# Optimization experiments

Measured on AMD Instinct MI355X. Metric: run time of the kernel, lower is better.

## Reference

```python
import jax, jax.numpy as jnp
import numpy as np

B, N, D = 64, 1024, 128
K = 6  # hardcoded neighbor count in the module


def setup_inputs() -> dict:
    key = jax.random.key(0)
    ks = jax.random.split(key, 11)
    def lin(k, out_d, in_d):
        kw, kb = jax.random.split(k)
        s = 1.0 / np.sqrt(in_d)
        W = jax.random.uniform(kw, (out_d, in_d), minval=-s, maxval=s, dtype=jnp.float32)
        b = jax.random.uniform(kb, (out_d,), minval=-s, maxval=s, dtype=jnp.float32)
        return W, b
    loc = jax.random.uniform(ks[0], (B, N, 2), dtype=jnp.float32)
    deadline = jax.random.uniform(ks[1], (B, N), dtype=jnp.float32)
    depot = jax.random.uniform(ks[2], (B, 2), dtype=jnp.float32)
    W3d, b3d = lin(ks[3], D, 3)
    W2d, b2d = lin(ks[4], D, 2)
    Wnb, bnb = lin(ks[5], D, K * D)
    Wdep, bdep = lin(ks[6], D, 2)
    return {"loc": loc, "deadline": deadline, "depot": depot,
            "W3d": W3d, "b3d": b3d, "W2d": W2d, "b2d": b2d,
            "Wnb": Wnb, "bnb": bnb, "Wdep": Wdep, "bdep": bdep}


def reference(loc, deadline, depot, W3d, b3d, W2d, b2d, Wnb, bnb, Wdep, bdep):
    x = jnp.concatenate([loc, deadline[:, :, None]], axis=2)  # [B,N,3]
    x2 = x[:, :, 0:2]                                          # [B,N,2]
    F2 = jnp.einsum('bnf,df->bnd', x2, W2d) + b2d              # [B,N,D]
    F3 = jnp.einsum('bnf,df->bnd', x, W3d) + b3d               # [B,N,D]
    # pairwise euclidean distances; indices are non-differentiable -> stop_gradient
    diff = x2[:, None, :, :] - x2[:, :, None, :]               # [B,N,N,2]
    dist = jnp.sqrt(jnp.sum(diff * diff, axis=-1))             # [B,N,N]
    _, neighbors = jax.lax.top_k(jax.lax.stop_gradient(-dist), K)  # [B,N,K] smallest dists (incl. self)
    # faithful quirk: original does F0_embedding_2d[:, neighbors][0] == gather from batch-0 embeddings
    nb = F2[0][neighbors]                                      # [B,N,K,D]
    nb_c = nb.reshape(nb.shape[0], nb.shape[1], K * nb.shape[3])  # [B,N,K*D]
    Fn = jnp.einsum('bnf,df->bnd', nb_c, Wnb) + bnb            # [B,N,D]
    Ff = Fn + F3
    dep = depot @ Wdep.T + bdep                                 # [B,D]
    h = jax.nn.leaky_relu(jnp.concatenate([dep[:, None, :], Ff], axis=1), negative_slope=0.01)
    return h, h.mean(axis=1)
```

## Files before the change

### kernel.cpp

```cpp
#include <hip/hip_runtime.h>
#include <hip/hip_bf16.h>

#define CB 64
#define CN 1024
#define CD 128
#define CK 6

typedef __attribute__((ext_vector_type(8))) short short8;
typedef __attribute__((ext_vector_type(4))) float floatx4;

__device__ __forceinline__ unsigned short f2bf(float f) {
    union { float f; unsigned u; } c; c.f = f;
    unsigned u = c.u;
    u += 0x7FFFu + ((u >> 16) & 1u);
    return (unsigned short)(u >> 16);
}

#define WS_F2B    0
#define WS_WNBB   262144
#define WS_PART   458752
#define WS_NBRS   983040
#define WS_IDS    1769472
#define WS_STARTS 1900544

__global__ void __launch_bounds__(256) k_grid(
    const float* __restrict__ loc,
    const float* __restrict__ W2d,
    const float* __restrict__ b2d,
    const float* __restrict__ Wnb,
    unsigned short* __restrict__ ids,
    int* __restrict__ starts,
    unsigned short* __restrict__ F2b,
    unsigned short* __restrict__ Wnbb)
{
    __shared__ float2 pts[CN];
    __shared__ int cnt[256];
    __shared__ int base[256];
    int b = blockIdx.x, t = threadIdx.x;
    const float2* lb = (const float2*)loc + b * CN;
#pragma unroll
    for (int r = 0; r < 4; ++r) pts[t + r * 256] = lb[t + r * 256];
    cnt[t] = 0;
    __syncthreads();
    int mycell[4];
#pragma unroll
    for (int r = 0; r < 4; ++r) {
        float2 p = pts[t * 4 + r];
        int cx = (int)(p.x * 16.0f); cx = cx > 15 ? 15 : cx;
        int cy = (int)(p.y * 16.0f); cy = cy > 15 ? 15 : cy;
        mycell[r] = (cy << 4) + cx;
        atomicAdd(&cnt[mycell[r]], 1);
    }
    __syncthreads();
    for (int off = 1; off < 256; off <<= 1) {
        int u = (t >= off) ? cnt[t - off] : 0;
        __syncthreads();
        cnt[t] += u;
        __syncthreads();
    }
    int excl = (t == 0) ? 0 : cnt[t - 1];
    base[t] = excl;
    starts[b * 257 + t] = excl;
    if (t == 255) starts[b * 257 + 256] = cnt[255];
    __syncthreads();
#pragma unroll
    for (int r = 0; r < 4; ++r) {
        int pos = atomicAdd(&base[mycell[r]], 1);
        ids[b * CN + pos] = (unsigned short)(t * 4 + r);
    }
#pragma unroll
    for (int e = 0; e < 8; ++e) {
        int idx = b * 2048 + e * 256 + t;
        int n = idx >> 7, d = idx & 127;
        float v = fmaf(loc[n * 2], W2d[d * 2],
                  fmaf(loc[n * 2 + 1], W2d[d * 2 + 1], b2d[d]));
        F2b[idx] = f2bf(v);
    }
#pragma unroll
    for (int e = 0; e < 6; ++e) {
        int idx = b * 1536 + e * 256 + t;
        Wnbb[idx] = f2bf(Wnb[idx]);
    }
}

__global__ void __launch_bounds__(256) k_knn(
    const float* __restrict__ loc,
    const unsigned short* __restrict__ ids,
    const int* __restrict__ starts,
    unsigned short* __restrict__ nbrs)
{
    __shared__ float2 xy_tmp[CN];
    __shared__ float2 xy_s[CN];
    __shared__ unsigned short ids_s[CN];
    __shared__ int st_s[257];
    int t = threadIdx.x;
    int b = blockIdx.x >> 2;
    int qbase = (blockIdx.x & 3) << 8;
    const float2* lb = (const float2*)loc + b * CN;
#pragma unroll
    for (int r = 0; r < 4; ++r) {
        int p = t + r * 256;
        xy_tmp[p] = lb[p];
        ids_s[p] = ids[b * CN + p];
    }
    st_s[t] = starts[b * 257 + t];
    if (t == 0) st_s[256] = starts[b * 257 + 256];
    __syncthreads();
#pragma unroll
    for (int r = 0; r < 4; ++r) {
        int p = t + r * 256;
        xy_s[p] = xy_tmp[ids_s[p]];
    }
    __syncthreads();

    int qp = qbase + t;
    int q = ids_s[qp];
    float2 qxy = xy_s[qp];
    float xq = qxy.x, yq = qxy.y;
    int cx = (int)(xq * 16.0f); cx = cx > 15 ? 15 : cx;
    int cy = (int)(yq * 16.0f); cy = cy > 15 ? 15 : cy;
    float dk[CK]; int ik[CK];
#pragma unroll
    for (int s = 0; s < CK; ++s) { dk[s] = 1e30f; ik[s] = 0x7FFFFFFF; }
    float dk5sq = __builtin_inff();
    const float h = 0.0625f;

#define KNN_CAND(P)                                                        \
    {                                                                      \
        float2 v = xy_s[P];                                                \
        float dx = __fsub_rn(v.x, xq);                                     \
        float dy = __fsub_rn(v.y, yq);                                     \
        float d2 = __fadd_rn(__fmul_rn(dx, dx), __fmul_rn(dy, dy));        \
        if (d2 < dk5sq) {                                                  \
            float ds = __fsqrt_rn(d2);                                     \
            int j = ids_s[P];                                              \
            if (ds < dk[CK - 1] || (ds == dk[CK - 1] && j < ik[CK - 1])) { \
                float dc = ds; int jc = j;                                 \
                _Pragma("unroll")                                          \
                for (int s = 0; s < CK; ++s) {                             \
                    bool sw = (dc < dk[s]) || (dc == dk[s] && jc < ik[s]); \
                    float od = dk[s]; int oi = ik[s];                      \
                    dk[s] = sw ? dc : od; ik[s] = sw ? jc : oi;            \
                    dc = sw ? od : dc;    jc = sw ? oi : jc;               \
                }                                                          \
                if (ik[CK - 1] != 0x7FFFFFFF)                              \
                    dk5sq = __fmul_rn(dk[CK - 1], dk[CK - 1]) * 1.000001f; \
            }                                                              \
        }                                                                  \
    }

    {
        int yl = cy > 0 ? cy - 1 : 0, yh = cy < 15 ? cy + 1 : 15;
        int xl = cx > 0 ? cx - 1 : 0, xh = cx < 15 ? cx + 1 : 15;
        for (int yy = yl; yy <= yh; ++yy) {
            int p  = st_s[(yy << 4) + xl];
            int pe = st_s[(yy << 4) + xh + 1];
            for (; p < pe; ++p) KNN_CAND(p)
        }
    }
    bool done;
    {
        int x0 = cx - 1, x1 = cx + 1, y0 = cy - 1, y1 = cy + 1;
        done = (x0 <= 0 && y0 <= 0 && x1 >= 15 && y1 >= 15);
        float mL = x0 > 0  ? __fsub_rn(xq, (float)x0 * h)       : 1e30f;
        float mR = x1 < 15 ? __fsub_rn((float)(x1 + 1) * h, xq) : 1e30f;
        float mB = y0 > 0  ? __fsub_rn(yq, (float)y0 * h)       : 1e30f;
        float mT = y1 < 15 ? __fsub_rn((float)(y1 + 1) * h, yq) : 1e30f;
        float bound = fminf(fminf(mL, mR), fminf(mB, mT)) * 0.999999f;
        done = done || (ik[CK - 1] != 0x7FFFFFFF && dk[CK - 1] < bound);
    }
    if (!done) {
        for (int r = 2; r < 16; ++r) {
            int x0 = cx - r, x1 = cx + r, y0 = cy - r, y1 = cy + r;
            int yl = y0 < 0 ? 0 : y0, yh = y1 > 15 ? 15 : y1;
            int xl = x0 < 0 ? 0 : x0, xh = x1 > 15 ? 15 : x1;
            for (int yy = yl; yy <= yh; ++yy) {
                bool ey = (yy == y0) || (yy == y1);
                if (ey) {
                    int p  = st_s[(yy << 4) + xl];
                    int pe = st_s[(yy << 4) + xh + 1];
                    for (; p < pe; ++p) KNN_CAND(p)
                } else {
                    if (x0 >= 0) {
                        int p  = st_s[(yy << 4) + x0];
                        int pe = st_s[(yy << 4) + x0 + 1];
                        for (; p < pe; ++p) KNN_CAND(p)
                    }
                    if (x1 <= 15) {
                        int p  = st_s[(yy << 4) + x1];
                        int pe = st_s[(yy << 4) + x1 + 1];
                        for (; p < pe; ++p) KNN_CAND(p)
                    }
                }
            }
            if (x0 <= 0 && y0 <= 0 && x1 >= 15 && y1 >= 15) break;
            float mL = x0 > 0  ? __fsub_rn(xq, (float)x0 * h)       : 1e30f;
            float mR = x1 < 15 ? __fsub_rn((float)(x1 + 1) * h, xq) : 1e30f;
            float mB = y0 > 0  ? __fsub_rn(yq, (float)y0 * h)       : 1e30f;
            float mT = y1 < 15 ? __fsub_rn((float)(y1 + 1) * h, yq) : 1e30f;
            float bound = fminf(fminf(mL, mR), fminf(mB, mT)) * 0.999999f;
            if (ik[CK - 1] != 0x7FFFFFFF && dk[CK - 1] < bound) break;
        }
    }
#undef KNN_CAND
    unsigned short* o = nbrs + (unsigned)(b * CN + q) * CK;
#pragma unroll
    for (int s = 0; s < CK; ++s) o[s] = (unsigned short)ik[s];
}

__global__ void __launch_bounds__(256) k_gemm(
    const float* __restrict__ loc,
    const float* __restrict__ dl,
    const unsigned short* __restrict__ F2b,
    const unsigned short* __restrict__ Wnbb,
    const unsigned short* __restrict__ nbrs,
    const float* __restrict__ bnb,
    const float* __restrict__ W3d,
    const float* __restrict__ b3d,
    float* __restrict__ outh,
    float* __restrict__ partials)
{
    __shared__ unsigned short As[128 * 40];
    __shared__ unsigned short Bs[128 * 40];
    __shared__ float psum[4][CD];

    int t = threadIdx.x;
    int rowbase = blockIdx.x * 128;
    int bb = rowbase >> 10;

    int ar0 = t >> 2, aseg = t & 3;
    int nb0[CK], nb1[CK];
#pragma unroll
    for (int s = 0; s < CK; ++s) {
        nb0[s] = (int)nbrs[(rowbase + ar0) * CK + s];
        nb1[s] = (int)nbrs[(rowbase + ar0 + 64) * CK + s];
    }

    int wave = t >> 6, lane = t & 63;
    int koff = (lane >> 4) * 8;
    int mrow = lane & 15;
    int bd = t >> 1, bhalf = t & 1;

    floatx4 acc[2][8];
#pragma unroll
    for (int i = 0; i < 2; ++i)
#pragma unroll
        for (int j = 0; j < 8; ++j) acc[i][j] = (floatx4){0.f, 0.f, 0.f, 0.f};

#pragma unroll
    for (int c = 0; c < 24; ++c) {
        const int kk = c >> 2;
        const int inner = (c & 3) * 32;
        __syncthreads();
        *(uint4*)&As[ar0 * 40 + aseg * 8] =
            *(const uint4*)(F2b + nb0[kk] * 128 + inner + aseg * 8);
        *(uint4*)&As[(ar0 + 64) * 40 + aseg * 8] =
            *(const uint4*)(F2b + nb1[kk] * 128 + inner + aseg * 8);
        {
            const uint4* src = (const uint4*)(Wnbb + bd * 768 + c * 32 + bhalf * 16);
            *(uint4*)&Bs[bd * 40 + bhalf * 16] = src[0];
            *(uint4*)&Bs[bd * 40 + bhalf * 16 + 8] = src[1];
        }
        __syncthreads();
        short8 af[2];
#pragma unroll
        for (int i = 0; i < 2; ++i)
            af[i] = *(const short8*)&As[(wave * 32 + i * 16 + mrow) * 40 + koff];
#pragma unroll
        for (int j = 0; j < 8; ++j) {
            short8 bfr = *(const short8*)&Bs[(j * 16 + mrow) * 40 + koff];
#pragma unroll
            for (int i = 0; i < 2; ++i)
                acc[i][j] = __builtin_amdgcn_mfma_f32_16x16x32_bf16(
                    af[i], bfr, acc[i][j], 0, 0, 0);
        }
    }

    int lq = lane >> 4, lc = lane & 15;
    float rl0[8], rl1[8], rdl[8]; int rn[8];
#pragma unroll
    for (int ir = 0; ir < 8; ++ir) {
        int i = ir >> 2, r = ir & 3;
        int mg = rowbase + wave * 32 + i * 16 + lq * 4 + r;
        float2 l2 = ((const float2*)loc)[mg];
        rl0[ir] = l2.x; rl1[ir] = l2.y; rdl[ir] = dl[mg];
        rn[ir] = mg & 1023;
    }
#pragma unroll
    for (int j = 0; j < 8; ++j) {
        int d = j * 16 + lc;
        float w0 = W3d[d * 3], w1 = W3d[d * 3 + 1], w2 = W3d[d * 3 + 2];
        float bias = b3d[d] + bnb[d];
        float csum = 0.f;
#pragma unroll
        for (int ir = 0; ir < 8; ++ir) {
            int i = ir >> 2, r = ir & 3;
            float v = acc[i][j][r] + bias + rl0[ir] * w0 + rl1[ir] * w1 + rdl[ir] * w2;
            float lr = v >= 0.f ? v : 0.01f * v;
            outh[((long)bb * 1025 + rn[ir] + 1) * 128 + d] = lr;
            csum += lr;
        }
        csum += __shfl_xor(csum, 16);
        csum += __shfl_xor(csum, 32);
        if (lq == 0) psum[wave][d] = csum;
    }
    __syncthreads();
    if (t < CD)
        partials[blockIdx.x * 128 + t] =
            psum[0][t] + psum[1][t] + psum[2][t] + psum[3][t];
}

__global__ void k_fin(const float* __restrict__ depot,
                      const float* __restrict__ Wdep,
                      const float* __restrict__ bdep,
                      const float* __restrict__ partials,
                      float* __restrict__ out) {
    int idx = blockIdx.x * 256 + threadIdx.x;
    int b = idx >> 7, d = idx & 127;
    float acc = 0.f;
#pragma unroll
    for (int g = 0; g < 8; ++g) acc += partials[(b * 8 + g) * 128 + d];
    float dv = depot[b * 2] * Wdep[d * 2] + depot[b * 2 + 1] * Wdep[d * 2 + 1] + bdep[d];
    float lr = dv >= 0.f ? dv : 0.01f * dv;
    out[(long)b * 1025 * 128 + d] = lr;
    out[(long)CB * 1025 * 128 + idx] = (acc + lr) * (1.0f / 1025.0f);
}

extern "C" void kernel_launch(void* const* d_in, const int* in_sizes, int n_in,
                              void* d_out, int out_size, void* d_ws, size_t ws_size,
                              hipStream_t stream) {
    const float* loc      = (const float*)d_in[0];
    const float* deadline = (const float*)d_in[1];
    const float* depot    = (const float*)d_in[2];
    const float* W3d      = (const float*)d_in[3];
    const float* b3d      = (const float*)d_in[4];
    const float* W2d      = (const float*)d_in[5];
    const float* b2d      = (const float*)d_in[6];
    const float* Wnb      = (const float*)d_in[7];
    const float* bnb      = (const float*)d_in[8];
    const float* Wdep     = (const float*)d_in[9];
    const float* bdep     = (const float*)d_in[10];
    float* out = (float*)d_out;

    char* ws = (char*)d_ws;
    unsigned short* F2b   = (unsigned short*)(ws + WS_F2B);
    unsigned short* Wnbb  = (unsigned short*)(ws + WS_WNBB);
    float* partials       = (float*)(ws + WS_PART);
    unsigned short* nbrs  = (unsigned short*)(ws + WS_NBRS);
    unsigned short* ids   = (unsigned short*)(ws + WS_IDS);
    int* starts           = (int*)(ws + WS_STARTS);

    k_grid<<<64, 256, 0, stream>>>(loc, W2d, b2d, Wnb, ids, starts, F2b, Wnbb);
    k_knn<<<256, 256, 0, stream>>>(loc, ids, starts, nbrs);
    k_gemm<<<512, 256, 0, stream>>>(loc, deadline, F2b, Wnbb, nbrs, bnb,
                                    W3d, b3d, out, partials);
    k_fin<<<32, 256, 0, stream>>>(depot, Wdep, bdep, partials, out);
}
```

Measured before the change: 142.9 us.

## Split each kNN query across four lanes and merge top-k via shuffles

Each query point is now handled by four threads rather than one. Each thread scans every fourth candidate in the grid cells and keeps its own top-6, and the four partial lists are merged with xor shuffles. The grid grows from 256 to 1024 blocks to raise occupancy and parallelism on the kNN search. The cost is that every block reloads the whole batch's coordinates into shared memory, each lane prunes with a weaker per-lane bound, lanes may expand to different search rings, and there is extra merge work.

```diff
diff --git a/kernel.cpp b/kernel.cpp
--- a/kernel.cpp
+++ b/kernel.cpp
@@ -94,8 +94,8 @@
     __shared__ unsigned short ids_s[CN];
     __shared__ int st_s[257];
     int t = threadIdx.x;
-    int b = blockIdx.x >> 2;
-    int qbase = (blockIdx.x & 3) << 8;
+    int b = blockIdx.x >> 4;
+    int qbase = (blockIdx.x & 15) << 6;
     const float2* lb = (const float2*)loc + b * CN;
 #pragma unroll
     for (int r = 0; r < 4; ++r) {
@@ -113,7 +113,8 @@
     }
     __syncthreads();
 
-    int qp = qbase + t;
+    int qp = qbase + (t >> 2);
+    int pi = t & 3;
     int q = ids_s[qp];
     float2 qxy = xy_s[qp];
     float xq = qxy.x, yq = qxy.y;
@@ -153,9 +154,9 @@
         int yl = cy > 0 ? cy - 1 : 0, yh = cy < 15 ? cy + 1 : 15;
         int xl = cx > 0 ? cx - 1 : 0, xh = cx < 15 ? cx + 1 : 15;
         for (int yy = yl; yy <= yh; ++yy) {
-            int p  = st_s[(yy << 4) + xl];
+            int p  = st_s[(yy << 4) + xl] + pi;
             int pe = st_s[(yy << 4) + xh + 1];
-            for (; p < pe; ++p) KNN_CAND(p)
+            for (; p < pe; p += 4) KNN_CAND(p)
         }
     }
     bool done;
@@ -177,19 +178,19 @@
             for (int yy = yl; yy <= yh; ++yy) {
                 bool ey = (yy == y0) || (yy == y1);
                 if (ey) {
-                    int p  = st_s[(yy << 4) + xl];
+                    int p  = st_s[(yy << 4) + xl] + pi;
                     int pe = st_s[(yy << 4) + xh + 1];
-                    for (; p < pe; ++p) KNN_CAND(p)
+                    for (; p < pe; p += 4) KNN_CAND(p)
                 } else {
                     if (x0 >= 0) {
-                        int p  = st_s[(yy << 4) + x0];
+                        int p  = st_s[(yy << 4) + x0] + pi;
                         int pe = st_s[(yy << 4) + x0 + 1];
-                        for (; p < pe; ++p) KNN_CAND(p)
+                        for (; p < pe; p += 4) KNN_CAND(p)
                     }
                     if (x1 <= 15) {
-                        int p  = st_s[(yy << 4) + x1];
+                        int p  = st_s[(yy << 4) + x1] + pi;
                         int pe = st_s[(yy << 4) + x1 + 1];
-                        for (; p < pe; ++p) KNN_CAND(p)
+                        for (; p < pe; p += 4) KNN_CAND(p)
                     }
                 }
             }
@@ -203,9 +204,38 @@
         }
     }
 #undef KNN_CAND
-    unsigned short* o = nbrs + (unsigned)(b * CN + q) * CK;
-#pragma unroll
-    for (int s = 0; s < CK; ++s) o[s] = (unsigned short)ik[s];
+
+#define KNN_MERGE(MASK)                                                     \
+    {                                                                       \
+        float od[CK]; int oi[CK];                                           \
+        _Pragma("unroll")                                                   \
+        for (int s = 0; s < CK; ++s) {                                      \
+            od[s] = __shfl_xor(dk[s], MASK);                                \
+            oi[s] = __shfl_xor(ik[s], MASK);                                \
+        }                                                                   \
+        _Pragma("unroll")                                                   \
+        for (int e = 0; e < CK; ++e) {                                      \
+            float dc = od[e]; int jc = oi[e];                               \
+            if ((dc < dk[CK - 1]) || (dc == dk[CK - 1] && jc < ik[CK - 1])) { \
+                _Pragma("unroll")                                           \
+                for (int s = 0; s < CK; ++s) {                              \
+                    bool sw = (dc < dk[s]) || (dc == dk[s] && jc < ik[s]);  \
+                    float td = dk[s]; int ti = ik[s];                       \
+                    dk[s] = sw ? dc : td; ik[s] = sw ? jc : ti;             \
+                    dc = sw ? td : dc;    jc = sw ? ti : jc;                \
+                }                                                           \
+            }                                                               \
+        }                                                                   \
+    }
+    KNN_MERGE(1)
+    KNN_MERGE(2)
+#undef KNN_MERGE
+
+    if (pi == 0) {
+        unsigned short* o = nbrs + (unsigned)(b * CN + q) * CK;
+#pragma unroll
+        for (int s = 0; s < CK; ++s) o[s] = (unsigned short)ik[s];
+    }
 }
 
 __global__ void __launch_bounds__(256) k_gemm(
@@ -351,7 +381,7 @@
     int* starts           = (int*)(ws + WS_STARTS);
 
     k_grid<<<64, 256, 0, stream>>>(loc, W2d, b2d, Wnb, ids, starts, F2b, Wnbb);
-    k_knn<<<256, 256, 0, stream>>>(loc, ids, starts, nbrs);
+    k_knn<<<1024, 256, 0, stream>>>(loc, ids, starts, nbrs);
     k_gemm<<<512, 256, 0, stream>>>(loc, deadline, F2b, Wnbb, nbrs, bnb,
                                     W3d, b3d, out, partials);
     k_fin<<<32, 256, 0, stream>>>(depot, Wdep, bdep, partials, out);
```

New measurement: 139.3 us. 1.03x faster.
